# Kernel optimization log

Measured on AMD Instinct MI355X. Metric: run time of the kernel, lower is better.

Reference implementation:

```python
import jax, jax.numpy as jnp
import numpy as np

N = 40000   # nodes
E = 600000  # edges
F = 128     # feature_size
H = 128     # hidden_channels
G = 32      # graphs in batch
C = 6       # classes


def setup_inputs() -> dict:
    key = jax.random.key(0)
    ks = jax.random.split(key, 20)
    x = jax.random.normal(ks[0], (N, F), jnp.float32)
    edge_index = jax.random.randint(ks[1], (2, E), 0, N, jnp.int32)
    batch = jnp.sort(jax.random.randint(ks[2], (N,), 0, G, jnp.int32))

    def lin_w(k, fan_in, fan_out):
        return jax.random.uniform(k, (fan_in, fan_out), jnp.float32,
                                  -1.0, 1.0) / np.sqrt(fan_in)

    inp = {"x": x, "edge_index": edge_index, "batch": batch,
           # GraphConv1: feature_size -> hidden (root + rel weights, bias)
           "w1_root": lin_w(ks[3], F, H), "w1_rel": lin_w(ks[4], F, H),
           "b1": jnp.zeros((H,), jnp.float32),
           # GraphConv2: hidden -> hidden
           "w2_root": lin_w(ks[5], H, H), "w2_rel": lin_w(ks[6], H, H),
           "b2": jnp.zeros((H,), jnp.float32),
           # GCNConv 3..5
           "w3": lin_w(ks[7], H, H), "b3": jnp.zeros((H,), jnp.float32),
           "w4": lin_w(ks[8], H, H), "b4": jnp.zeros((H,), jnp.float32),
           "w5": lin_w(ks[9], H, H), "b5": jnp.zeros((H,), jnp.float32),
           # final Linear(hidden, 6)
           "lin_w": lin_w(ks[10], H, C), "lin_b": jnp.zeros((C,), jnp.float32)}
    return inp


def _graph_conv(x, w_root, w_rel, b, src, dst, n):
    # PyG GraphConv (aggr='add'): out_i = W_root x_i + W_rel * sum_{j->i} x_j + b
    agg = jax.ops.segment_sum(x[src], dst, num_segments=n)
    return agg @ w_rel + x @ w_root + b


def _gcn_conv(x, w, b, src_sl, dst_sl, deg_inv_sqrt, n):
    # PyG GCNConv: out = D^-1/2 (A+I) D^-1/2 (X W) + b
    h = x @ w
    norm = deg_inv_sqrt[src_sl] * deg_inv_sqrt[dst_sl]  # [E+N]
    out = jax.ops.segment_sum(h[src_sl] * norm[:, None], dst_sl, num_segments=n)
    return out + b


def reference(x, edge_index, batch, w1_root, w1_rel, b1, w2_root, w2_rel, b2,
              w3, b3, w4, b4, w5, b5, lin_w, lin_b):
    src, dst = edge_index[0], edge_index[1]
    # self-loops for GCN layers
    loop = jnp.arange(N, dtype=edge_index.dtype)
    src_sl = jnp.concatenate([src, loop])
    dst_sl = jnp.concatenate([dst, loop])
    deg = jax.ops.segment_sum(jnp.ones((E + N,), x.dtype), dst_sl, num_segments=N)
    deg_inv_sqrt = jax.lax.rsqrt(deg)  # deg >= 1 due to self-loops

    h = jax.nn.relu(_graph_conv(x, w1_root, w1_rel, b1, src, dst, N))
    h = jax.nn.relu(_graph_conv(h, w2_root, w2_rel, b2, src, dst, N))
    h = jax.nn.relu(_gcn_conv(h, w3, b3, src_sl, dst_sl, deg_inv_sqrt, N))
    h = jax.nn.relu(_gcn_conv(h, w4, b4, src_sl, dst_sl, deg_inv_sqrt, N))
    h = _gcn_conv(h, w5, b5, src_sl, dst_sl, deg_inv_sqrt, N)

    # global_mean_pool over batch assignment
    counts = jax.ops.segment_sum(jnp.ones((N,), h.dtype), batch, num_segments=G)
    sums = jax.ops.segment_sum(h, batch, num_segments=G)
    embedding = sums / jnp.maximum(counts, 1.0)[:, None]  # [G, H]

    # dropout p=0.5 is identity in eval mode
    logits = embedding @ lin_w + lin_b  # [G, C]
    return (logits, embedding)
```

## Files before the change

kernel.cpp:

```cpp
#include <hip/hip_runtime.h>
#include <hip/hip_fp8.h>

#define Nn 40000
#define Ee 600000
#define Hh 128
#define Gg 32
#define Cc 6
#define CAP 64
#define NT (Nn / 16)
#define LSTR 136
#define PADW 0x9C409C40u

typedef __bf16 bf16x8 __attribute__((ext_vector_type(8)));
typedef float floatx4 __attribute__((ext_vector_type(4)));
typedef float floatx2 __attribute__((ext_vector_type(2)));
typedef unsigned short u16;
typedef unsigned int u32;
typedef unsigned char u8;

__device__ __forceinline__ u16 f2b(float f) {
    union { float f; u32 i; } v; v.f = f;
    u32 r = v.i + 0x7fffu + ((v.i >> 16) & 1u);
    return (u16)(r >> 16);
}
__device__ __forceinline__ u32 pack2(float a, float b) {
    return (u32)f2b(a) | ((u32)f2b(b) << 16);
}
__device__ __forceinline__ u8 f8e(float f) {
    __hip_fp8_e4m3 v(f); return (u8)v.__x;
}
__device__ __forceinline__ u8 f8e_hw(float f) {
    return (u8)(__builtin_amdgcn_cvt_pk_fp8_f32(f, f, 0, false) & 0xff);
}

__global__ __launch_bounds__(256) void k_setup(int* cursor, float* emb,
                                               u16* xb, u16* hA16, u8* xf8, u8* hA8, u8* hB8,
                                               float* dinv, u16* colidx,
                                               const float* __restrict__ x,
                                               const float* w0, const float* w1, const float* w2,
                                               const float* w3, const float* w4, const float* w5,
                                               const float* w6, u16* __restrict__ pwdst) {
    int gid = blockIdx.x * 256 + threadIdx.x;
    if (gid < Nn) cursor[gid] = 0;
    if (gid < Gg * Hh) emb[gid] = 0.f;
    if (blockIdx.x == 0) {
        int t = threadIdx.x;
        uint4 z = { 0, 0, 0, 0 };
        if (t < 16)              *(uint4*)(xb  + (size_t)Nn * 128 + t * 8) = z;
        else if (t < 32)         *(uint4*)(hA16 + (size_t)Nn * 128 + (t - 16) * 8) = z;
        else if (t < 40)         *(uint4*)(xf8 + (size_t)Nn * 128 + (t - 32) * 16) = z;
        else if (t < 48)         *(uint4*)(hA8 + (size_t)Nn * 128 + (t - 40) * 16) = z;
        else if (t < 56)         *(uint4*)(hB8 + (size_t)Nn * 128 + (t - 48) * 16) = z;
        else if (t == 56)        dinv[Nn] = 0.f;
    }
    if (blockIdx.x < 448) {
        int idx = gid;
        if (idx < 7 * 16384) {
            const float* ws[7] = { w0, w1, w2, w3, w4, w5, w6 };
            int mat = idx >> 14, r = idx & 16383;
            int j = r & 7, n = (r >> 3) & 15, q = (r >> 7) & 3, nt = (r >> 9) & 7, t = r >> 12;
            pwdst[idx] = f2b(ws[mat][(t * 32 + q * 8 + j) * 128 + nt * 16 + n]);
        }
    } else {
        int gid2 = (blockIdx.x - 448) * 256 + threadIdx.x;
        int i = gid2 * 4;
        float4 v = *(const float4*)(x + i);
        ushort4 o = { f2b(v.x), f2b(v.y), f2b(v.z), f2b(v.w) };
        *(ushort4*)(xb + i) = o;
        u32 p8 = (u32)f8e(v.x) | ((u32)f8e(v.y) << 8) | ((u32)f8e(v.z) << 16) | ((u32)f8e(v.w) << 24);
        *(u32*)(xf8 + i) = p8;
        *(u32*)(colidx + gid2 * 2) = PADW;
    }
}

__global__ __launch_bounds__(256) void k_scatter(const int* __restrict__ src, const int* __restrict__ dst,
                                                 int* __restrict__ cursor, u16* __restrict__ colidx) {
    int i = blockIdx.x * 256 + threadIdx.x;
    if (i < Ee) {
        int d = dst[i];
        int p = atomicAdd(&cursor[d], 1);
        if (p < CAP) colidx[d * CAP + p] = (u16)src[i];
    }
}

#define UPC_ADD(V) { floatx2 p_;                                                          \
    p_ = __builtin_amdgcn_cvt_pk_f32_fp8((int)(V).x, false); a0 += p_.x; a1 += p_.y;      \
    p_ = __builtin_amdgcn_cvt_pk_f32_fp8((int)(V).x, true);  a2 += p_.x; a3 += p_.y;      \
    p_ = __builtin_amdgcn_cvt_pk_f32_fp8((int)(V).y, false); a4 += p_.x; a5 += p_.y;      \
    p_ = __builtin_amdgcn_cvt_pk_f32_fp8((int)(V).y, true);  a6 += p_.x; a7 += p_.y; }

__global__ __launch_bounds__(256) void k_layer(const u8* __restrict__ hin8,
                                               const u16* __restrict__ hin16,
                                               const u16* __restrict__ Bp_agg,
                                               const u16* __restrict__ Bp_self,
                                               const float* __restrict__ bias,
                                               u16* __restrict__ hout16,
                                               u8* __restrict__ hout8,
                                               const int* __restrict__ cursor,
                                               const u16* __restrict__ pcol,
                                               float* __restrict__ dinv,
                                               const int* __restrict__ batch,
                                               float* __restrict__ emb,
                                               int gcn, int relu, int dopool, int wrdinv, int scale8) {
    __shared__ u16 Asm[16 * LSTR];
    __shared__ float Psm[16][132];
    int wave = threadIdx.x >> 6, lane = threadIdx.x & 63;
    int m0 = blockIdx.x * 16;

    {
        int g = lane >> 4, l = lane & 15;
        int nloc = wave * 4 + g;
        int node = m0 + nloc;
        int c = cursor[node]; if (c > CAP) c = CAP;
        if (wrdinv && l == 0) dinv[node] = rsqrtf((float)(c + 1));
        int beg = node * CAP;
        int end = beg + ((c + 7) & ~7);
        float a0 = 0.f, a1 = 0.f, a2 = 0.f, a3 = 0.f, a4 = 0.f, a5 = 0.f, a6 = 0.f, a7 = 0.f;
        const u8* b8 = hin8 + l * 8;
        if (beg < end) {
            uint4 ip = *(const uint4*)(pcol + beg);
            for (int e = beg; e < end; e += 8) {
                int en = (e + 8 < end) ? (e + 8) : beg;
                uint4 jp = *(const uint4*)(pcol + en);
                u32 e0 = ip.x & 0xFFFFu, e1 = ip.x >> 16;
                u32 e2 = ip.y & 0xFFFFu, e3 = ip.y >> 16;
                u32 e4 = ip.z & 0xFFFFu, e5 = ip.z >> 16;
                u32 e6 = ip.w & 0xFFFFu, e7 = ip.w >> 16;
                uint2 v0 = *(const uint2*)(b8 + (size_t)e0 * 128);
                uint2 v1 = *(const uint2*)(b8 + (size_t)e1 * 128);
                uint2 v2 = *(const uint2*)(b8 + (size_t)e2 * 128);
                uint2 v3 = *(const uint2*)(b8 + (size_t)e3 * 128);
                uint2 v4 = *(const uint2*)(b8 + (size_t)e4 * 128);
                uint2 v5 = *(const uint2*)(b8 + (size_t)e5 * 128);
                uint2 v6 = *(const uint2*)(b8 + (size_t)e6 * 128);
                uint2 v7 = *(const uint2*)(b8 + (size_t)e7 * 128);
                UPC_ADD(v0) UPC_ADD(v1) UPC_ADD(v2) UPC_ADD(v3)
                UPC_ADD(v4) UPC_ADD(v5) UPC_ADD(v6) UPC_ADD(v7)
                ip = jp;
            }
        }
        if (gcn) {
            uint2 us = *(const uint2*)(b8 + (size_t)node * 128);
            UPC_ADD(us)
            float di = dinv[node];
            a0 *= di; a1 *= di; a2 *= di; a3 *= di;
            a4 *= di; a5 *= di; a6 *= di; a7 *= di;
        }
        uint4 o = { pack2(a0, a1), pack2(a2, a3), pack2(a4, a5), pack2(a6, a7) };
        *(uint4*)&Asm[nloc * LSTR + l * 8] = o;
    }
    __syncthreads();

    {
        int n = lane & 15, q = lane >> 4;
        floatx4 acc0 = (floatx4){0.f, 0.f, 0.f, 0.f};
        floatx4 acc1 = (floatx4){0.f, 0.f, 0.f, 0.f};
        int nt0 = wave * 2, nt1 = wave * 2 + 1;
#pragma unroll
        for (int t = 0; t < 4; t++) {
            bf16x8 a = *(const bf16x8*)&Asm[n * LSTR + q * 8 + t * 32];
            const u16* bp = Bp_agg + t * 4096 + q * 128 + n * 8;
            bf16x8 b0 = *(const bf16x8*)(bp + nt0 * 512);
            bf16x8 b1 = *(const bf16x8*)(bp + nt1 * 512);
            acc0 = __builtin_amdgcn_mfma_f32_16x16x32_bf16(a, b0, acc0, 0, 0, 0);
            acc1 = __builtin_amdgcn_mfma_f32_16x16x32_bf16(a, b1, acc1, 0, 0, 0);
        }
        if (!gcn) {
            const u16* arow = hin16 + (size_t)(m0 + n) * 128 + q * 8;
#pragma unroll
            for (int t = 0; t < 4; t++) {
                bf16x8 a = *(const bf16x8*)(arow + t * 32);
                const u16* bp = Bp_self + t * 4096 + q * 128 + n * 8;
                bf16x8 b0 = *(const bf16x8*)(bp + nt0 * 512);
                bf16x8 b1 = *(const bf16x8*)(bp + nt1 * 512);
                acc0 = __builtin_amdgcn_mfma_f32_16x16x32_bf16(a, b0, acc0, 0, 0, 0);
                acc1 = __builtin_amdgcn_mfma_f32_16x16x32_bf16(a, b1, acc1, 0, 0, 0);
            }
        }
        if (dopool) {
#pragma unroll
            for (int j = 0; j < 2; j++) {
                int col = (wave * 2 + j) * 16 + n;
                float bv = bias[col];
                floatx4 ac = j ? acc1 : acc0;
#pragma unroll
                for (int r = 0; r < 4; r++)
                    Psm[q * 4 + r][col] = ac[r] + bv;
            }
            __syncthreads();
            if (threadIdx.x < 128) {
                int col = threadIdx.x;
                int g0 = batch[m0], g1 = batch[m0 + 15];
                for (int g = g0; g <= g1; ++g) {
                    float s = 0.f;
#pragma unroll
                    for (int i = 0; i < 16; ++i)
                        if (batch[m0 + i] == g) s += Psm[i][col];
                    atomicAdd(&emb[g * 128 + col], s);
                }
            }
        } else {
            float sc[4];
#pragma unroll
            for (int r = 0; r < 4; r++)
                sc[r] = scale8 ? dinv[m0 + q * 4 + r] : 1.f;
#pragma unroll
            for (int j = 0; j < 2; j++) {
                int col = (wave * 2 + j) * 16 + n;
                float bv = bias[col];
                floatx4 ac = j ? acc1 : acc0;
#pragma unroll
                for (int r = 0; r < 4; r++) {
                    float v = ac[r] + bv;
                    if (relu) v = fmaxf(v, 0.f);
                    size_t idx = (size_t)(m0 + q * 4 + r) * 128 + col;
                    if (hout16) hout16[idx] = f2b(v);
                    if (hout8)  hout8[idx]  = f8e_hw(v * sc[r]);
                }
            }
        }
    }
}

__global__ __launch_bounds__(256) void k_final(const float* __restrict__ emb, const int* __restrict__ batch,
                                               const float* __restrict__ lw, const float* __restrict__ lb,
                                               float* __restrict__ out) {
    __shared__ float cnt[Gg];
    int t = threadIdx.x;
    if (t < Gg) {
        int lo = 0, hi = Nn;
        while (lo < hi) { int m = (lo + hi) >> 1; if (batch[m] < t) lo = m + 1; else hi = m; }
        int lb0 = lo;
        lo = 0; hi = Nn;
        int tg = t + 1;
        while (lo < hi) { int m = (lo + hi) >> 1; if (batch[m] < tg) lo = m + 1; else hi = m; }
        cnt[t] = fmaxf((float)(lo - lb0), 1.f);
    }
    __syncthreads();
    for (int i = t; i < Gg * Hh; i += 256) {
        int g = i >> 7;
        out[Gg * Cc + i] = emb[i] / cnt[g];
    }
    if (t < Gg * Cc) {
        int g = t / Cc, c = t % Cc;
        float cn = cnt[g];
        float s = lb[c];
        for (int f = 0; f < Hh; f++)
            s += (emb[g * 128 + f] / cn) * lw[f * Cc + c];
        out[t] = s;
    }
}

extern "C" void kernel_launch(void* const* d_in, const int* in_sizes, int n_in,
                              void* d_out, int out_size, void* d_ws, size_t ws_size,
                              hipStream_t stream) {
    const float* x       = (const float*)d_in[0];
    const int*   ei      = (const int*)d_in[1];
    const int*   batch   = (const int*)d_in[2];
    const float* w1_root = (const float*)d_in[3];
    const float* w1_rel  = (const float*)d_in[4];
    const float* b1      = (const float*)d_in[5];
    const float* w2_root = (const float*)d_in[6];
    const float* w2_rel  = (const float*)d_in[7];
    const float* b2      = (const float*)d_in[8];
    const float* w3      = (const float*)d_in[9];
    const float* b3      = (const float*)d_in[10];
    const float* w4      = (const float*)d_in[11];
    const float* b4      = (const float*)d_in[12];
    const float* w5      = (const float*)d_in[13];
    const float* b5      = (const float*)d_in[14];
    const float* lw      = (const float*)d_in[15];
    const float* lb      = (const float*)d_in[16];
    const int* srcp = ei;
    const int* dstp = ei + Ee;
    float* out = (float*)d_out;

    char* w = (char*)d_ws;
    size_t off = 0;
    auto alloc = [&](size_t bytes) { size_t r = off; off += (bytes + 255) & ~(size_t)255; return r; };
    int*   cursor  = (int*)(w + alloc(Nn * 4));
    u16*   colidx  = (u16*)(w + alloc((size_t)Nn * CAP * 2));
    float* dinv    = (float*)(w + alloc((Nn + 1) * 4));
    float* emb     = (float*)(w + alloc(Gg * Hh * 4));
    u16*   pw      = (u16*)(w + alloc(7 * 16384 * 2));
    u16*   xb      = (u16*)(w + alloc((size_t)(Nn + 1) * Hh * 2));
    u16*   hA16    = (u16*)(w + alloc((size_t)(Nn + 1) * Hh * 2));
    u8*    xf8     = (u8*)(w + alloc((size_t)(Nn + 1) * Hh));
    u8*    hA8     = (u8*)(w + alloc((size_t)(Nn + 1) * Hh));
    u8*    hB8     = (u8*)(w + alloc((size_t)(Nn + 1) * Hh));
    (void)ws_size;

    u16* pw1r = pw + 0 * 16384;
    u16* pw1l = pw + 1 * 16384;
    u16* pw2r = pw + 2 * 16384;
    u16* pw2l = pw + 3 * 16384;
    u16* pw3  = pw + 4 * 16384;
    u16* pw4  = pw + 5 * 16384;
    u16* pw5  = pw + 6 * 16384;
    const u16* nil16 = (const u16*)nullptr;
    u16* no16 = (u16*)nullptr;
    u8*  no8  = (u8*)nullptr;

    hipLaunchKernelGGL(k_setup, dim3(448 + Nn * Hh / 1024), dim3(256), 0, stream,
                       cursor, emb, xb, hA16, xf8, hA8, hB8, dinv, colidx,
                       x, w1_root, w1_rel, w2_root, w2_rel, w3, w4, w5, pw);
    hipLaunchKernelGGL(k_scatter, dim3((Ee + 255) / 256), dim3(256), 0, stream,
                       srcp, dstp, cursor, colidx);

    hipLaunchKernelGGL(k_layer, dim3(NT), dim3(256), 0, stream,
                       xf8, xb, pw1l, pw1r, b1, hA16, hA8, cursor, colidx, dinv, batch, emb,
                       0, 1, 0, 1, 0);
    hipLaunchKernelGGL(k_layer, dim3(NT), dim3(256), 0, stream,
                       hA8, hA16, pw2l, pw2r, b2, no16, hB8, cursor, colidx, dinv, batch, emb,
                       0, 1, 0, 0, 1);
    hipLaunchKernelGGL(k_layer, dim3(NT), dim3(256), 0, stream,
                       hB8, nil16, pw3, nil16, b3, no16, hA8, cursor, colidx, dinv, batch, emb,
                       1, 1, 0, 0, 1);
    hipLaunchKernelGGL(k_layer, dim3(NT), dim3(256), 0, stream,
                       hA8, nil16, pw4, nil16, b4, no16, xf8, cursor, colidx, dinv, batch, emb,
                       1, 1, 0, 0, 1);
    hipLaunchKernelGGL(k_layer, dim3(NT), dim3(256), 0, stream,
                       xf8, nil16, pw5, nil16, b5, no16, no8, cursor, colidx, dinv, batch, emb,
                       1, 0, 1, 0, 0);

    hipLaunchKernelGGL(k_final, dim3(1), dim3(256), 0, stream, emb, batch, lw, lb, out);
}
```

Baseline: 249.9 us.

## Make layer kernel persistent with atomic work-stealing over node tiles

Each layer kernel now launches a fixed grid of 2048 blocks that repeatedly claim 16-node tiles through an atomic counter, replacing the one-block-per-tile launch of 2500 blocks. The counters are zeroed in the setup kernel, one per layer. The goal is to balance uneven degree-dependent gather work and cut block launch overhead. In exchange it adds an atomic and extra barriers per tile, and with 2048 blocks against 2500 tiles most blocks process only one or two tiles.

```diff
diff --git a/kernel.cpp b/kernel.cpp
--- a/kernel.cpp
+++ b/kernel.cpp
@@ -10,6 +10,7 @@
 #define NT (Nn / 16)
 #define LSTR 136
 #define PADW 0x9C409C40u
+#define LGRID 2048
 
 typedef __bf16 bf16x8 __attribute__((ext_vector_type(8)));
 typedef float floatx4 __attribute__((ext_vector_type(4)));
@@ -33,7 +34,7 @@
     return (u8)(__builtin_amdgcn_cvt_pk_fp8_f32(f, f, 0, false) & 0xff);
 }
 
-__global__ __launch_bounds__(256) void k_setup(int* cursor, float* emb,
+__global__ __launch_bounds__(256) void k_setup(int* cursor, float* emb, int* wctr,
                                                u16* xb, u16* hA16, u8* xf8, u8* hA8, u8* hB8,
                                                float* dinv, u16* colidx,
                                                const float* __restrict__ x,
@@ -43,6 +44,7 @@
     int gid = blockIdx.x * 256 + threadIdx.x;
     if (gid < Nn) cursor[gid] = 0;
     if (gid < Gg * Hh) emb[gid] = 0.f;
+    if (gid < 8) wctr[gid] = 0;
     if (blockIdx.x == 0) {
         int t = threadIdx.x;
         uint4 z = { 0, 0, 0, 0 };
@@ -101,124 +103,134 @@
                                                float* __restrict__ dinv,
                                                const int* __restrict__ batch,
                                                float* __restrict__ emb,
+                                               int* __restrict__ wctr,
                                                int gcn, int relu, int dopool, int wrdinv, int scale8) {
     __shared__ u16 Asm[16 * LSTR];
     __shared__ float Psm[16][132];
+    __shared__ int s_tile;
     int wave = threadIdx.x >> 6, lane = threadIdx.x & 63;
-    int m0 = blockIdx.x * 16;
-
-    {
-        int g = lane >> 4, l = lane & 15;
-        int nloc = wave * 4 + g;
-        int node = m0 + nloc;
-        int c = cursor[node]; if (c > CAP) c = CAP;
-        if (wrdinv && l == 0) dinv[node] = rsqrtf((float)(c + 1));
-        int beg = node * CAP;
-        int end = beg + ((c + 7) & ~7);
-        float a0 = 0.f, a1 = 0.f, a2 = 0.f, a3 = 0.f, a4 = 0.f, a5 = 0.f, a6 = 0.f, a7 = 0.f;
-        const u8* b8 = hin8 + l * 8;
-        if (beg < end) {
-            uint4 ip = *(const uint4*)(pcol + beg);
-            for (int e = beg; e < end; e += 8) {
-                int en = (e + 8 < end) ? (e + 8) : beg;
-                uint4 jp = *(const uint4*)(pcol + en);
-                u32 e0 = ip.x & 0xFFFFu, e1 = ip.x >> 16;
-                u32 e2 = ip.y & 0xFFFFu, e3 = ip.y >> 16;
-                u32 e4 = ip.z & 0xFFFFu, e5 = ip.z >> 16;
-                u32 e6 = ip.w & 0xFFFFu, e7 = ip.w >> 16;
-                uint2 v0 = *(const uint2*)(b8 + (size_t)e0 * 128);
-                uint2 v1 = *(const uint2*)(b8 + (size_t)e1 * 128);
-                uint2 v2 = *(const uint2*)(b8 + (size_t)e2 * 128);
-                uint2 v3 = *(const uint2*)(b8 + (size_t)e3 * 128);
-                uint2 v4 = *(const uint2*)(b8 + (size_t)e4 * 128);
-                uint2 v5 = *(const uint2*)(b8 + (size_t)e5 * 128);
-                uint2 v6 = *(const uint2*)(b8 + (size_t)e6 * 128);
-                uint2 v7 = *(const uint2*)(b8 + (size_t)e7 * 128);
-                UPC_ADD(v0) UPC_ADD(v1) UPC_ADD(v2) UPC_ADD(v3)
-                UPC_ADD(v4) UPC_ADD(v5) UPC_ADD(v6) UPC_ADD(v7)
-                ip = jp;
-            }
+
+    for (;;) {
+        if (threadIdx.x == 0) s_tile = atomicAdd(wctr, 1);
+        __syncthreads();
+        int tile = s_tile;
+        if (tile >= NT) break;
+        int m0 = tile * 16;
+
+        {
+            int g = lane >> 4, l = lane & 15;
+            int nloc = wave * 4 + g;
+            int node = m0 + nloc;
+            int c = cursor[node]; if (c > CAP) c = CAP;
+            if (wrdinv && l == 0) dinv[node] = rsqrtf((float)(c + 1));
+            int beg = node * CAP;
+            int end = beg + ((c + 7) & ~7);
+            float a0 = 0.f, a1 = 0.f, a2 = 0.f, a3 = 0.f, a4 = 0.f, a5 = 0.f, a6 = 0.f, a7 = 0.f;
+            const u8* b8 = hin8 + l * 8;
+            if (beg < end) {
+                uint4 ip = *(const uint4*)(pcol + beg);
+                for (int e = beg; e < end; e += 8) {
+                    int en = (e + 8 < end) ? (e + 8) : beg;
+                    uint4 jp = *(const uint4*)(pcol + en);
+                    u32 e0 = ip.x & 0xFFFFu, e1 = ip.x >> 16;
+                    u32 e2 = ip.y & 0xFFFFu, e3 = ip.y >> 16;
+                    u32 e4 = ip.z & 0xFFFFu, e5 = ip.z >> 16;
+                    u32 e6 = ip.w & 0xFFFFu, e7 = ip.w >> 16;
+                    uint2 v0 = *(const uint2*)(b8 + (size_t)e0 * 128);
+                    uint2 v1 = *(const uint2*)(b8 + (size_t)e1 * 128);
+                    uint2 v2 = *(const uint2*)(b8 + (size_t)e2 * 128);
+                    uint2 v3 = *(const uint2*)(b8 + (size_t)e3 * 128);
+                    uint2 v4 = *(const uint2*)(b8 + (size_t)e4 * 128);
+                    uint2 v5 = *(const uint2*)(b8 + (size_t)e5 * 128);
+                    uint2 v6 = *(const uint2*)(b8 + (size_t)e6 * 128);
+                    uint2 v7 = *(const uint2*)(b8 + (size_t)e7 * 128);
+                    UPC_ADD(v0) UPC_ADD(v1) UPC_ADD(v2) UPC_ADD(v3)
+                    UPC_ADD(v4) UPC_ADD(v5) UPC_ADD(v6) UPC_ADD(v7)
+                    ip = jp;
+                }
+            }
+            if (gcn) {
+                uint2 us = *(const uint2*)(b8 + (size_t)node * 128);
+                UPC_ADD(us)
+                float di = dinv[node];
+                a0 *= di; a1 *= di; a2 *= di; a3 *= di;
+                a4 *= di; a5 *= di; a6 *= di; a7 *= di;
+            }
+            uint4 o = { pack2(a0, a1), pack2(a2, a3), pack2(a4, a5), pack2(a6, a7) };
+            *(uint4*)&Asm[nloc * LSTR + l * 8] = o;
         }
-        if (gcn) {
-            uint2 us = *(const uint2*)(b8 + (size_t)node * 128);
-            UPC_ADD(us)
-            float di = dinv[node];
-            a0 *= di; a1 *= di; a2 *= di; a3 *= di;
-            a4 *= di; a5 *= di; a6 *= di; a7 *= di;
-        }
-        uint4 o = { pack2(a0, a1), pack2(a2, a3), pack2(a4, a5), pack2(a6, a7) };
-        *(uint4*)&Asm[nloc * LSTR + l * 8] = o;
-    }
-    __syncthreads();
-
-    {
-        int n = lane & 15, q = lane >> 4;
-        floatx4 acc0 = (floatx4){0.f, 0.f, 0.f, 0.f};
-        floatx4 acc1 = (floatx4){0.f, 0.f, 0.f, 0.f};
-        int nt0 = wave * 2, nt1 = wave * 2 + 1;
-#pragma unroll
-        for (int t = 0; t < 4; t++) {
-            bf16x8 a = *(const bf16x8*)&Asm[n * LSTR + q * 8 + t * 32];
-            const u16* bp = Bp_agg + t * 4096 + q * 128 + n * 8;
-            bf16x8 b0 = *(const bf16x8*)(bp + nt0 * 512);
-            bf16x8 b1 = *(const bf16x8*)(bp + nt1 * 512);
-            acc0 = __builtin_amdgcn_mfma_f32_16x16x32_bf16(a, b0, acc0, 0, 0, 0);
-            acc1 = __builtin_amdgcn_mfma_f32_16x16x32_bf16(a, b1, acc1, 0, 0, 0);
-        }
-        if (!gcn) {
-            const u16* arow = hin16 + (size_t)(m0 + n) * 128 + q * 8;
+        __syncthreads();
+
+        {
+            int n = lane & 15, q = lane >> 4;
+            floatx4 acc0 = (floatx4){0.f, 0.f, 0.f, 0.f};
+            floatx4 acc1 = (floatx4){0.f, 0.f, 0.f, 0.f};
+            int nt0 = wave * 2, nt1 = wave * 2 + 1;
 #pragma unroll
             for (int t = 0; t < 4; t++) {
-                bf16x8 a = *(const bf16x8*)(arow + t * 32);
-                const u16* bp = Bp_self + t * 4096 + q * 128 + n * 8;
+                bf16x8 a = *(const bf16x8*)&Asm[n * LSTR + q * 8 + t * 32];
+                const u16* bp = Bp_agg + t * 4096 + q * 128 + n * 8;
                 bf16x8 b0 = *(const bf16x8*)(bp + nt0 * 512);
                 bf16x8 b1 = *(const bf16x8*)(bp + nt1 * 512);
                 acc0 = __builtin_amdgcn_mfma_f32_16x16x32_bf16(a, b0, acc0, 0, 0, 0);
                 acc1 = __builtin_amdgcn_mfma_f32_16x16x32_bf16(a, b1, acc1, 0, 0, 0);
             }
+            if (!gcn) {
+                const u16* arow = hin16 + (size_t)(m0 + n) * 128 + q * 8;
+#pragma unroll
+                for (int t = 0; t < 4; t++) {
+                    bf16x8 a = *(const bf16x8*)(arow + t * 32);
+                    const u16* bp = Bp_self + t * 4096 + q * 128 + n * 8;
+                    bf16x8 b0 = *(const bf16x8*)(bp + nt0 * 512);
+                    bf16x8 b1 = *(const bf16x8*)(bp + nt1 * 512);
+                    acc0 = __builtin_amdgcn_mfma_f32_16x16x32_bf16(a, b0, acc0, 0, 0, 0);
+                    acc1 = __builtin_amdgcn_mfma_f32_16x16x32_bf16(a, b1, acc1, 0, 0, 0);
+                }
+            }
+            if (dopool) {
+#pragma unroll
+                for (int j = 0; j < 2; j++) {
+                    int col = (wave * 2 + j) * 16 + n;
+                    float bv = bias[col];
+                    floatx4 ac = j ? acc1 : acc0;
+#pragma unroll
+                    for (int r = 0; r < 4; r++)
+                        Psm[q * 4 + r][col] = ac[r] + bv;
+                }
+                __syncthreads();
+                if (threadIdx.x < 128) {
+                    int col = threadIdx.x;
+                    int g0 = batch[m0], g1 = batch[m0 + 15];
+                    for (int g = g0; g <= g1; ++g) {
+                        float s = 0.f;
+#pragma unroll
+                        for (int i = 0; i < 16; ++i)
+                            if (batch[m0 + i] == g) s += Psm[i][col];
+                        atomicAdd(&emb[g * 128 + col], s);
+                    }
+                }
+            } else {
+                float sc[4];
+#pragma unroll
+                for (int r = 0; r < 4; r++)
+                    sc[r] = scale8 ? dinv[m0 + q * 4 + r] : 1.f;
+#pragma unroll
+                for (int j = 0; j < 2; j++) {
+                    int col = (wave * 2 + j) * 16 + n;
+                    float bv = bias[col];
+                    floatx4 ac = j ? acc1 : acc0;
+#pragma unroll
+                    for (int r = 0; r < 4; r++) {
+                        float v = ac[r] + bv;
+                        if (relu) v = fmaxf(v, 0.f);
+                        size_t idx = (size_t)(m0 + q * 4 + r) * 128 + col;
+                        if (hout16) hout16[idx] = f2b(v);
+                        if (hout8)  hout8[idx]  = f8e_hw(v * sc[r]);
+                    }
+                }
+            }
         }
-        if (dopool) {
-#pragma unroll
-            for (int j = 0; j < 2; j++) {
-                int col = (wave * 2 + j) * 16 + n;
-                float bv = bias[col];
-                floatx4 ac = j ? acc1 : acc0;
-#pragma unroll
-                for (int r = 0; r < 4; r++)
-                    Psm[q * 4 + r][col] = ac[r] + bv;
-            }
-            __syncthreads();
-            if (threadIdx.x < 128) {
-                int col = threadIdx.x;
-                int g0 = batch[m0], g1 = batch[m0 + 15];
-                for (int g = g0; g <= g1; ++g) {
-                    float s = 0.f;
-#pragma unroll
-                    for (int i = 0; i < 16; ++i)
-                        if (batch[m0 + i] == g) s += Psm[i][col];
-                    atomicAdd(&emb[g * 128 + col], s);
-                }
-            }
-        } else {
-            float sc[4];
-#pragma unroll
-            for (int r = 0; r < 4; r++)
-                sc[r] = scale8 ? dinv[m0 + q * 4 + r] : 1.f;
-#pragma unroll
-            for (int j = 0; j < 2; j++) {
-                int col = (wave * 2 + j) * 16 + n;
-                float bv = bias[col];
-                floatx4 ac = j ? acc1 : acc0;
-#pragma unroll
-                for (int r = 0; r < 4; r++) {
-                    float v = ac[r] + bv;
-                    if (relu) v = fmaxf(v, 0.f);
-                    size_t idx = (size_t)(m0 + q * 4 + r) * 128 + col;
-                    if (hout16) hout16[idx] = f2b(v);
-                    if (hout8)  hout8[idx]  = f8e_hw(v * sc[r]);
-                }
-            }
-        }
+        __syncthreads();
     }
 }
 
@@ -282,6 +294,7 @@
     u16*   colidx  = (u16*)(w + alloc((size_t)Nn * CAP * 2));
     float* dinv    = (float*)(w + alloc((Nn + 1) * 4));
     float* emb     = (float*)(w + alloc(Gg * Hh * 4));
+    int*   wctr    = (int*)(w + alloc(256));
     u16*   pw      = (u16*)(w + alloc(7 * 16384 * 2));
     u16*   xb      = (u16*)(w + alloc((size_t)(Nn + 1) * Hh * 2));
     u16*   hA16    = (u16*)(w + alloc((size_t)(Nn + 1) * Hh * 2));
@@ -302,26 +315,26 @@
     u8*  no8  = (u8*)nullptr;
 
     hipLaunchKernelGGL(k_setup, dim3(448 + Nn * Hh / 1024), dim3(256), 0, stream,
-                       cursor, emb, xb, hA16, xf8, hA8, hB8, dinv, colidx,
+                       cursor, emb, wctr, xb, hA16, xf8, hA8, hB8, dinv, colidx,
                        x, w1_root, w1_rel, w2_root, w2_rel, w3, w4, w5, pw);
     hipLaunchKernelGGL(k_scatter, dim3((Ee + 255) / 256), dim3(256), 0, stream,
                        srcp, dstp, cursor, colidx);
 
-    hipLaunchKernelGGL(k_layer, dim3(NT), dim3(256), 0, stream,
+    hipLaunchKernelGGL(k_layer, dim3(LGRID), dim3(256), 0, stream,
                        xf8, xb, pw1l, pw1r, b1, hA16, hA8, cursor, colidx, dinv, batch, emb,
-                       0, 1, 0, 1, 0);
-    hipLaunchKernelGGL(k_layer, dim3(NT), dim3(256), 0, stream,
+                       wctr + 0, 0, 1, 0, 1, 0);
+    hipLaunchKernelGGL(k_layer, dim3(LGRID), dim3(256), 0, stream,
                        hA8, hA16, pw2l, pw2r, b2, no16, hB8, cursor, colidx, dinv, batch, emb,
-                       0, 1, 0, 0, 1);
-    hipLaunchKernelGGL(k_layer, dim3(NT), dim3(256), 0, stream,
+                       wctr + 1, 0, 1, 0, 0, 1);
+    hipLaunchKernelGGL(k_layer, dim3(LGRID), dim3(256), 0, stream,
                        hB8, nil16, pw3, nil16, b3, no16, hA8, cursor, colidx, dinv, batch, emb,
-                       1, 1, 0, 0, 1);
-    hipLaunchKernelGGL(k_layer, dim3(NT), dim3(256), 0, stream,
+                       wctr + 2, 1, 1, 0, 0, 1);
+    hipLaunchKernelGGL(k_layer, dim3(LGRID), dim3(256), 0, stream,
                        hA8, nil16, pw4, nil16, b4, no16, xf8, cursor, colidx, dinv, batch, emb,
-                       1, 1, 0, 0, 1);
-    hipLaunchKernelGGL(k_layer, dim3(NT), dim3(256), 0, stream,
+                       wctr + 3, 1, 1, 0, 0, 1);
+    hipLaunchKernelGGL(k_layer, dim3(LGRID), dim3(256), 0, stream,
                        xf8, nil16, pw5, nil16, b5, no16, no8, cursor, colidx, dinv, batch, emb,
-                       1, 0, 1, 0, 0);
+                       wctr + 4, 1, 0, 1, 0, 0);
 
     hipLaunchKernelGGL(k_final, dim3(1), dim3(256), 0, stream, emb, batch, lw, lb, out);
 }
```

Result: slower. 444.0 us (+77.7%).
